# Kernel tuning notes

Measured on AMD Instinct MI355X. Metric: run time of the kernel, lower is better.

Reference implementation:

```python
import jax, jax.numpy as jnp
import numpy as np

NUM_LAYERS = 32
IN_SIZE = 1024
OUT_SIZE = 1024
B, S = 32, 256


def setup_inputs() -> dict:
    key = jax.random.key(0)
    k1, k2, k3 = jax.random.split(key, 3)
    x = jax.random.normal(k1, (B, S, IN_SIZE), dtype=jnp.float32)
    layer_idx = jax.random.randint(k2, (S,), 0, NUM_LAYERS, dtype=jnp.int32)
    # learned parameter: per-layer weight [L, O, D], normal(stddev=1.0) as in flax init
    weight = jax.random.normal(k3, (NUM_LAYERS, OUT_SIZE, IN_SIZE), dtype=jnp.float32)
    return {"x": x, "layer_idx": layer_idx, "weight": weight}


def reference(x, layer_idx, weight):
    # x: [B, S, D]; layer_idx: [S]; weight: [L, O, D]
    # Each sequence position s uses expert weight[layer_idx[s]]:
    #   out[b, s, o] = sum_d x[b, s, d] * weight[layer_idx[s], o, d]
    w = weight[layer_idx]                      # [S, O, D] gather
    return jnp.einsum('bsd,sod->bso', x, w)    # [B, S, O]
```

## Files before the change

kernel.cpp:

```cpp
#include <hip/hip_runtime.h>
#include <hip/hip_bf16.h>
#include <stdint.h>

#define NLAYERS 32
#define DSIZE   1024
#define OSIZE   1024
#define BATCH   32
#define SEQ     256

#define WS_PERM  16
#define WS_TILE  512
#define MAX_TILES 88
#define NSPLIT   16

typedef __attribute__((ext_vector_type(8)))  short short8;
typedef __attribute__((ext_vector_type(16))) float f32x16;

#define LDSTRIDE 72
#define BK 64

static __device__ __forceinline__ void lds_barrier() {
    asm volatile("s_waitcnt lgkmcnt(0)\n\ts_barrier" ::: "memory");
}

__global__ void prep_kernel(const int* __restrict__ layer_idx, int* __restrict__ wsi) {
    __shared__ int cnt[NLAYERS];
    __shared__ int start_[NLAYERS];
    __shared__ int cursor[NLAYERS];
    const int t = threadIdx.x;
    if (t < NLAYERS) cnt[t] = 0;
    __syncthreads();
    int l = 0;
    if (t < SEQ) { l = layer_idx[t]; atomicAdd(&cnt[l], 1); }
    __syncthreads();
    if (t == 0) {
        int acc = 0;
        for (int i = 0; i < NLAYERS; ++i) { start_[i] = acc; cursor[i] = acc; acc += cnt[i]; }
    }
    __syncthreads();
    if (t < SEQ) {
        int r = atomicAdd(&cursor[l], 1);
        wsi[WS_PERM + r] = t;
    }
    if (t == 0) {
        int nt = 0;
        for (int i = 0; i < NLAYERS; ++i) {
            const int c = cnt[i];
            for (int j = 0; j < c; j += 4) {
                wsi[WS_TILE + nt*4 + 0] = i;
                wsi[WS_TILE + nt*4 + 1] = start_[i] + j;
                wsi[WS_TILE + nt*4 + 2] = (c - j < 4) ? (c - j) : 4;
                ++nt;
            }
        }
        wsi[0] = nt;
    }
}

static __device__ __forceinline__ unsigned pk2(float a, float b) {
    unsigned ua = __builtin_bit_cast(unsigned, a) + 0x8000u;
    unsigned ub = __builtin_bit_cast(unsigned, b) + 0x8000u;
    return __builtin_amdgcn_perm(ub, ua, 0x07060302u);
}

__global__ __launch_bounds__(256, 4) void gemm_kernel(
        const float* __restrict__ x, const float* __restrict__ wgt,
        const int* __restrict__ wsi, float* __restrict__ out) {
    const int ntiles = wsi[0];
    const int xcd = blockIdx.x & 7;
    const int idx = blockIdx.x >> 3;
    const int g_lo = (xcd * ntiles) >> 3;
    const int g_hi = ((xcd + 1) * ntiles) >> 3;
    const int nblk = (g_hi - g_lo) << 4;
    if (idx >= nblk) return;
    const int mt    = g_lo + (idx >> 4);
    const int ntile = idx & 15;
    const int layer     = wsi[WS_TILE + mt*4 + 0];
    const int rank_base = wsi[WS_TILE + mt*4 + 1];
    const int nranks    = wsi[WS_TILE + mt*4 + 2];

    __shared__ __align__(16) short ldsA[128 * LDSTRIDE];
    __shared__ __align__(16) short ldsB[64 * LDSTRIDE];

    const int t     = threadIdx.x;
    const int c4    = (t & 15) * 4;
    const int rbase = t >> 4;

    bool svalid[4];
    int  sv[4];
    #pragma unroll
    for (int j = 0; j < 4; ++j) {
        svalid[j] = (j < nranks);
        sv[j] = svalid[j] ? wsi[WS_PERM + rank_base + j] : 0;
    }

    const float* aptr[8];
    #pragma unroll
    for (int p = 0; p < 8; ++p) {
        const int roff = p >> 1;
        const int b    = rbase + ((p & 1) << 4);
        aptr[p] = x + (((size_t)(b * SEQ + sv[roff])) << 10) + c4;
    }
    const float* bbase = wgt + (((size_t)((layer << 10) + ntile * 64 + rbase)) << 10) + c4;

    float4 ra[8], rb[4];
    auto load_step = [&](int kk) {
        #pragma unroll
        for (int p = 0; p < 8; ++p) {
            if (svalid[p >> 1]) ra[p] = *(const float4*)(aptr[p] + kk);
            else                ra[p] = make_float4(0.f, 0.f, 0.f, 0.f);
        }
        #pragma unroll
        for (int p = 0; p < 4; ++p)
            rb[p] = *(const float4*)(bbase + ((size_t)p << 14) + kk);
    };

    const int lane = t & 63;
    const int wv   = t >> 6;
    const int wm   = wv * 32;
    const int l31  = lane & 31;
    const int lh   = lane >> 5;

    f32x16 acc[2];
    #pragma unroll
    for (int ni = 0; ni < 2; ++ni)
        #pragma unroll
        for (int r = 0; r < 16; ++r) acc[ni][r] = 0.f;

    const short* pA0 = &ldsA[(wm + l31) * LDSTRIDE + lh * 8];
    const short* pB0 = &ldsB[l31 * LDSTRIDE + lh * 8];

    load_step(0);
    #pragma unroll 1
    for (int kk = 0; kk < DSIZE; kk += BK) {
        lds_barrier();
        #pragma unroll
        for (int p = 0; p < 8; ++p) {
            const int row = rbase + 16 * p;
            uint2 va;
            va.x = pk2(ra[p].x, ra[p].y);
            va.y = pk2(ra[p].z, ra[p].w);
            *(uint2*)&ldsA[row * LDSTRIDE + c4] = va;
        }
        #pragma unroll
        for (int p = 0; p < 4; ++p) {
            const int row = rbase + 16 * p;
            uint2 vb;
            vb.x = pk2(rb[p].x, rb[p].y);
            vb.y = pk2(rb[p].z, rb[p].w);
            *(uint2*)&ldsB[row * LDSTRIDE + c4] = vb;
        }
        if (kk + BK < DSIZE) load_step(kk + BK);
        lds_barrier();
        #pragma unroll
        for (int sub = 0; sub < 4; ++sub) {
            short8 a0 = *(const short8*)(pA0 + sub*16);
            short8 b0 = *(const short8*)(pB0 + sub*16);
            short8 b1 = *(const short8*)(pB0 + 32*LDSTRIDE + sub*16);
            acc[0] = __builtin_amdgcn_mfma_f32_32x32x16_bf16(a0, b0, acc[0], 0, 0, 0);
            acc[1] = __builtin_amdgcn_mfma_f32_32x32x16_bf16(a0, b1, acc[1], 0, 0, 0);
        }
    }

    if (wv < nranks) {
        const int s = wsi[WS_PERM + rank_base + wv];
        #pragma unroll
        for (int ni = 0; ni < 2; ++ni) {
            const int ocol = ntile * 64 + ni * 32 + l31;
            #pragma unroll
            for (int r = 0; r < 16; ++r) {
                const int brow = (r & 3) + 8 * (r >> 2) + 4 * lh;
                out[(((size_t)(brow * SEQ + s)) << 10) + ocol] = acc[ni][r];
            }
        }
    }
}

extern "C" void kernel_launch(void* const* d_in, const int* in_sizes, int n_in,
                              void* d_out, int out_size, void* d_ws, size_t ws_size,
                              hipStream_t stream) {
    const float* x         = (const float*)d_in[0];
    const int*   layer_idx = (const int*)  d_in[1];
    const float* weight    = (const float*)d_in[2];
    float* out = (float*)d_out;
    int*   wsi = (int*)d_ws;

    prep_kernel<<<1, 256, 0, stream>>>(layer_idx, wsi);
    gemm_kernel<<<MAX_TILES * NSPLIT, 256, 0, stream>>>(x, weight, wsi, out);
}
```

Baseline: 252.3 us.

## Double block size to 512 threads with one 32x32 MFMA tile per wave

Each block now runs 8 waves instead of 4, and each wave computes a single 32x32 output tile (row group by N-half) instead of two. Per-thread global loads and LDS staging are halved and launch bounds rise to 512x7, aiming for more waves in flight to hide memory latency and fewer registers per thread. The trade-off is more waves sharing the same LDS tile and barriers, and less MFMA work per wave per A-fragment load.

```diff
diff --git a/kernel.cpp b/kernel.cpp
--- a/kernel.cpp
+++ b/kernel.cpp
@@ -1,5 +1,4 @@
 #include <hip/hip_runtime.h>
-#include <hip/hip_bf16.h>
 #include <stdint.h>
 
 #define NLAYERS 32
@@ -63,7 +62,7 @@
     return __builtin_amdgcn_perm(ub, ua, 0x07060302u);
 }
 
-__global__ __launch_bounds__(256, 4) void gemm_kernel(
+__global__ __launch_bounds__(512, 7) void gemm_kernel(
         const float* __restrict__ x, const float* __restrict__ wgt,
         const int* __restrict__ wsi, float* __restrict__ out) {
     const int ntiles = wsi[0];
@@ -86,65 +85,55 @@
     const int c4    = (t & 15) * 4;
     const int rbase = t >> 4;
 
-    bool svalid[4];
-    int  sv[4];
+    int sv[4];
     #pragma unroll
-    for (int j = 0; j < 4; ++j) {
-        svalid[j] = (j < nranks);
-        sv[j] = svalid[j] ? wsi[WS_PERM + rank_base + j] : 0;
-    }
+    for (int j = 0; j < 4; ++j)
+        sv[j] = (j < nranks) ? wsi[WS_PERM + rank_base + j] : 0;
 
-    const float* aptr[8];
-    #pragma unroll
-    for (int p = 0; p < 8; ++p) {
-        const int roff = p >> 1;
-        const int b    = rbase + ((p & 1) << 4);
-        aptr[p] = x + (((size_t)(b * SEQ + sv[roff])) << 10) + c4;
-    }
-    const float* bbase = wgt + (((size_t)((layer << 10) + ntile * 64 + rbase)) << 10) + c4;
+    const float* abase = x + (((size_t)(rbase * SEQ)) << 10) + c4;
+    const float* bptr = wgt + (((size_t)((layer << 10) + ntile * 64 + rbase)) << 10) + c4;
 
-    float4 ra[8], rb[4];
+    float4 ra[4], rb[2];
     auto load_step = [&](int kk) {
         #pragma unroll
-        for (int p = 0; p < 8; ++p) {
-            if (svalid[p >> 1]) ra[p] = *(const float4*)(aptr[p] + kk);
-            else                ra[p] = make_float4(0.f, 0.f, 0.f, 0.f);
+        for (int p = 0; p < 4; ++p) {
+            if (p < nranks) ra[p] = *(const float4*)(abase + ((size_t)sv[p] << 10) + kk);
+            else            ra[p] = make_float4(0.f, 0.f, 0.f, 0.f);
         }
         #pragma unroll
-        for (int p = 0; p < 4; ++p)
-            rb[p] = *(const float4*)(bbase + ((size_t)p << 14) + kk);
+        for (int p = 0; p < 2; ++p)
+            rb[p] = *(const float4*)(bptr + ((size_t)p << 15) + kk);
     };
 
     const int lane = t & 63;
     const int wv   = t >> 6;
-    const int wm   = wv * 32;
+    const int ro   = wv >> 1;
+    const int nh   = wv & 1;
     const int l31  = lane & 31;
     const int lh   = lane >> 5;
 
-    f32x16 acc[2];
+    f32x16 acc;
     #pragma unroll
-    for (int ni = 0; ni < 2; ++ni)
-        #pragma unroll
-        for (int r = 0; r < 16; ++r) acc[ni][r] = 0.f;
+    for (int r = 0; r < 16; ++r) acc[r] = 0.f;
 
-    const short* pA0 = &ldsA[(wm + l31) * LDSTRIDE + lh * 8];
-    const short* pB0 = &ldsB[l31 * LDSTRIDE + lh * 8];
+    const short* pA0 = &ldsA[(ro * 32 + l31) * LDSTRIDE + lh * 8];
+    const short* pB0 = &ldsB[(nh * 32 + l31) * LDSTRIDE + lh * 8];
 
     load_step(0);
     #pragma unroll 1
     for (int kk = 0; kk < DSIZE; kk += BK) {
         lds_barrier();
         #pragma unroll
-        for (int p = 0; p < 8; ++p) {
-            const int row = rbase + 16 * p;
+        for (int p = 0; p < 4; ++p) {
+            const int row = rbase + 32 * p;
             uint2 va;
             va.x = pk2(ra[p].x, ra[p].y);
             va.y = pk2(ra[p].z, ra[p].w);
             *(uint2*)&ldsA[row * LDSTRIDE + c4] = va;
         }
         #pragma unroll
-        for (int p = 0; p < 4; ++p) {
-            const int row = rbase + 16 * p;
+        for (int p = 0; p < 2; ++p) {
+            const int row = rbase + 32 * p;
             uint2 vb;
             vb.x = pk2(rb[p].x, rb[p].y);
             vb.y = pk2(rb[p].z, rb[p].w);
@@ -156,22 +145,17 @@
         for (int sub = 0; sub < 4; ++sub) {
             short8 a0 = *(const short8*)(pA0 + sub*16);
             short8 b0 = *(const short8*)(pB0 + sub*16);
-            short8 b1 = *(const short8*)(pB0 + 32*LDSTRIDE + sub*16);
-            acc[0] = __builtin_amdgcn_mfma_f32_32x32x16_bf16(a0, b0, acc[0], 0, 0, 0);
-            acc[1] = __builtin_amdgcn_mfma_f32_32x32x16_bf16(a0, b1, acc[1], 0, 0, 0);
+            acc = __builtin_amdgcn_mfma_f32_32x32x16_bf16(a0, b0, acc, 0, 0, 0);
         }
     }
 
-    if (wv < nranks) {
-        const int s = wsi[WS_PERM + rank_base + wv];
+    if (ro < nranks) {
+        const int s = wsi[WS_PERM + rank_base + ro];
+        const int ocol = ntile * 64 + nh * 32 + l31;
         #pragma unroll
-        for (int ni = 0; ni < 2; ++ni) {
-            const int ocol = ntile * 64 + ni * 32 + l31;
-            #pragma unroll
-            for (int r = 0; r < 16; ++r) {
-                const int brow = (r & 3) + 8 * (r >> 2) + 4 * lh;
-                out[(((size_t)(brow * SEQ + s)) << 10) + ocol] = acc[ni][r];
-            }
+        for (int r = 0; r < 16; ++r) {
+            const int brow = (r & 3) + 8 * (r >> 2) + 4 * lh;
+            out[(((size_t)(brow * SEQ + s)) << 10) + ocol] = acc[r];
         }
     }
 }
@@ -186,5 +170,5 @@
     int*   wsi = (int*)d_ws;
 
     prep_kernel<<<1, 256, 0, stream>>>(layer_idx, wsi);
-    gemm_kernel<<<MAX_TILES * NSPLIT, 256, 0, stream>>>(x, weight, wsi, out);
+    gemm_kernel<<<MAX_TILES * NSPLIT, 512, 0, stream>>>(x, weight, wsi, out);
 }
```

After: 259.5 us. 2.9% more time.
